# Performance work log

Hardware: AMD Instinct MI355X
Metric: run time of the kernel (lower is better)

The kernel has to match this reference:

```python
import jax, jax.numpy as jnp
import numpy as np

N = 100_000   # nodes
D = 64        # hidden = H * C
H, C = 8, 8   # heads, per-head channels
E = 500_000   # edges per edge set
EPS = 1e-3    # keras LayerNormalization default epsilon
RSQRT_C = np.float32(1.0 / np.sqrt(C))


def setup_inputs() -> dict:
    key = jax.random.key(0)
    ks = jax.random.split(key, 13)
    s = 0.05
    return dict(
        x=jax.random.normal(ks[0], (N, D), jnp.float32),
        src0=jax.random.randint(ks[1], (E,), 0, N, jnp.int32),
        dst0=jax.random.randint(ks[2], (E,), 0, N, jnp.int32),
        src1=jax.random.randint(ks[3], (E,), 0, N, jnp.int32),
        dst1=jax.random.randint(ks[4], (E,), 0, N, jnp.int32),
        Wk=jax.random.normal(ks[5], (D, D), jnp.float32) * s,
        bk=jnp.zeros((D,), jnp.float32),
        Wm=jax.random.normal(ks[6], (D, D), jnp.float32) * s,
        bm=jnp.zeros((D,), jnp.float32),
        Wq=jax.random.normal(ks[7], (D, D), jnp.float32) * s,
        bq=jnp.zeros((D,), jnp.float32),
        Wa=jax.random.normal(ks[8], (D, D), jnp.float32) * s,
        ba=jnp.zeros((D,), jnp.float32),
        Watt0=jax.random.normal(ks[9], (H, C, C), jnp.float32) * s,
        Wmsg0=jax.random.normal(ks[10], (H, C, C), jnp.float32) * s,
        prior0=jnp.ones((H,), jnp.float32),
        Watt1=jax.random.normal(ks[11], (H, C, C), jnp.float32) * s,
        Wmsg1=jax.random.normal(ks[12], (H, C, C), jnp.float32) * s,
        prior1=jnp.ones((H,), jnp.float32),
        skip_w=jnp.ones((1,), jnp.float32),
        ln_gamma=jnp.ones((D,), jnp.float32),
        ln_beta=jnp.zeros((D,), jnp.float32),
    )


def _edge_terms(k, m, q, src, dst, Watt, Wmsg, prior):
    # gather sender keys/messages, apply per-edge-set per-head projections
    ke = jnp.einsum('ehk,hkl->ehl', k[src], Watt)          # [E,H,C]
    score = jnp.einsum('ehc,ehc->eh', ke, q[dst]) * prior * RSQRT_C  # [E,H]
    me = jnp.einsum('ehk,hkl->ehl', m[src], Wmsg)          # [E,H,C]
    return score, me


def _forward(x, src0, dst0, src1, dst1, Wk, bk, Wm, bm, Wq, bq, Wa, ba,
             Watt0, Wmsg0, prior0, Watt1, Wmsg1, prior1,
             skip_w, ln_gamma, ln_beta):
    n = x.shape[0]
    split = lambda t: t.reshape(n, H, C)
    k = split(x @ Wk + bk)   # sender keys   [N,H,C]
    m = split(x @ Wm + bm)   # sender msgs   [N,H,C]
    q = split(x @ Wq + bq)   # receiver qrys [N,H,C]

    s0, m0 = _edge_terms(k, m, q, src0, dst0, Watt0, Wmsg0, prior0)
    s1, m1 = _edge_terms(k, m, q, src1, dst1, Watt1, Wmsg1, prior1)

    # joint segment softmax over ALL incoming edges per receiver (across edge sets)
    scores = jnp.concatenate([s0, s1], axis=0)  # [Et,H]
    msgs = jnp.concatenate([m0, m1], axis=0)    # [Et,H,C]
    recv = jnp.concatenate([dst0, dst1], axis=0)
    smax = jax.ops.segment_max(scores, recv, num_segments=n)
    ex = jnp.exp(scores - smax[recv])
    denom = jax.ops.segment_sum(ex, recv, num_segments=n)
    coef = ex / denom[recv]                      # [Et,H]

    pooled = jax.ops.segment_sum(coef[:, :, None] * msgs, recv, num_segments=n)  # [N,H,C]
    merged = pooled.reshape(n, D)
    agg = jax.nn.gelu(merged, approximate=False) @ Wa + ba
    # (dropout_rate=0.0 -> identity)
    sc = jax.nn.sigmoid(skip_w[0])               # learnable weighted skip
    out = sc * agg + (1.0 - sc) * x
    # layer norm (keras default eps=1e-3)
    mu = jnp.mean(out, axis=-1, keepdims=True)
    var = jnp.var(out, axis=-1, keepdims=True)
    return ln_gamma * (out - mu) * jax.lax.rsqrt(var + EPS) + ln_beta


def reference(x, src0, dst0, src1, dst1, Wk, bk, Wm, bm, Wq, bq, Wa, ba,
              Watt0, Wmsg0, prior0, Watt1, Wmsg1, prior1,
              skip_w, ln_gamma, ln_beta):
    return _forward(x, src0, dst0, src1, dst1, Wk, bk, Wm, bm, Wq, bq, Wa, ba,
                    Watt0, Wmsg0, prior0, Watt1, Wmsg1, prior1,
                    skip_w, ln_gamma, ln_beta)
```

## Files before the change

kernel.cpp:

```cpp
#include <hip/hip_runtime.h>
#include <hip/hip_fp16.h>
#include <cstdint>
#include <cstddef>

#define TPB 256
static constexpr float RSQRT_C_F = 0.35355339059327373f;

typedef __attribute__((ext_vector_type(8))) short bf16x8;
typedef __attribute__((ext_vector_type(4))) float f32x4;
typedef __attribute__((ext_vector_type(2))) float f32x2;

#if __has_builtin(__builtin_amdgcn_cvt_pk_f32_fp8) && __has_builtin(__builtin_amdgcn_cvt_pk_fp8_f32)
#define USE_HW_FP8 1
#endif

__device__ __forceinline__ unsigned short f2bf(float f) {
    unsigned u = __float_as_uint(f);
    u += 0x7FFFu + ((u >> 16) & 1u);
    return (unsigned short)(u >> 16);
}
__device__ __forceinline__ float bf2f(unsigned short h) {
    return __uint_as_float((unsigned)h << 16);
}
__device__ __forceinline__ float loF(unsigned u) { return __uint_as_float(u << 16); }
__device__ __forceinline__ float hiF(unsigned u) { return __uint_as_float(u); }

__device__ __forceinline__ unsigned char enc8(float v) {
#ifdef USE_HW_FP8
    return (unsigned char)(__builtin_amdgcn_cvt_pk_fp8_f32(v, v, 0, false) & 0xff);
#else
    unsigned s = (__float_as_uint(v) >> 24) & 0x80u;
    float a = fabsf(v);
    if (a < 0.015625f) {
        int m = __float2int_rn(a * 512.f);
        return (unsigned char)(s | (unsigned)m);
    }
    if (a > 448.f) return (unsigned char)(s | 0x7e);
    unsigned u = __float_as_uint(a);
    u += 0x7FFFFu + ((u >> 20) & 1u);
    unsigned e8 = ((u >> 23) & 0xffu) - 120u;
    unsigned m3 = (u >> 20) & 7u;
    if (e8 > 15u) return (unsigned char)(s | 0x7e);
    return (unsigned char)(s | (e8 << 3) | m3);
#endif
}

__device__ __forceinline__ void dec8x8(uint2 v, float* o) {
#ifdef USE_HW_FP8
    f32x2 a = __builtin_amdgcn_cvt_pk_f32_fp8((int)v.x, false);
    f32x2 b = __builtin_amdgcn_cvt_pk_f32_fp8((int)v.x, true);
    f32x2 c = __builtin_amdgcn_cvt_pk_f32_fp8((int)v.y, false);
    f32x2 d = __builtin_amdgcn_cvt_pk_f32_fp8((int)v.y, true);
    o[0] = a.x; o[1] = a.y; o[2] = b.x; o[3] = b.y;
    o[4] = c.x; o[5] = c.y; o[6] = d.x; o[7] = d.y;
#else
    unsigned w[2] = {v.x, v.y};
    #pragma unroll
    for (int i = 0; i < 8; i++) {
        unsigned bb = (w[i >> 2] >> ((i & 3) * 8)) & 0xffu;
        unsigned short hs = (unsigned short)(((bb & 0x80u) << 8) | ((bb & 0x7fu) << 7));
        __half h = *reinterpret_cast<__half*>(&hs);
        o[i] = 256.f * __half2float(h);
    }
#endif
}

__global__ void zero_sub(int4* __restrict__ p, int n4) {
    int i = blockIdx.x * TPB + threadIdx.x;
    int stride = gridDim.x * TPB;
    for (; i < n4; i += stride) p[i] = int4{0, 0, 0, 0};
}

__global__ void prep1_kernel(const float* __restrict__ Wq, const float* __restrict__ bq,
                             const float* __restrict__ Wk, const float* __restrict__ bk,
                             const float* __restrict__ Wm, const float* __restrict__ bm,
                             const float* __restrict__ Watt0, const float* __restrict__ prior0,
                             const float* __restrict__ Watt1, const float* __restrict__ prior1,
                             const float* __restrict__ Wmsg0, const float* __restrict__ Wmsg1,
                             float* __restrict__ Wbig, float* __restrict__ bbig) {
    int idx = blockIdx.x * TPB + threadIdx.x;
    if (idx < 64 * 320) {
        int i = idx / 320, col = idx % 320;
        float v;
        if (col < 64) {
            v = Wq[i * 64 + col];
        } else {
            int j = col - 64, set = j >> 6, l = j & 63, h = l >> 3, lc = l & 7;
            const float* Win = (set < 2) ? Wk : Wm;
            const float* T = (set == 0) ? Watt0 : (set == 1) ? Watt1 : (set == 2) ? Wmsg0 : Wmsg1;
            float scale = (set == 0) ? prior0[h] * RSQRT_C_F
                        : (set == 1) ? prior1[h] * RSQRT_C_F : 1.f;
            float acc = 0.f;
            #pragma unroll
            for (int c = 0; c < 8; c++) acc += Win[i * 64 + h * 8 + c] * T[h * 64 + c * 8 + lc];
            v = acc * scale;
        }
        Wbig[idx] = v;
    } else if (idx < 64 * 320 + 320) {
        int col = idx - 64 * 320;
        float v;
        if (col < 64) {
            v = bq[col];
        } else {
            int j = col - 64, set = j >> 6, l = j & 63, h = l >> 3, lc = l & 7;
            const float* bin = (set < 2) ? bk : bm;
            const float* T = (set == 0) ? Watt0 : (set == 1) ? Watt1 : (set == 2) ? Wmsg0 : Wmsg1;
            float scale = (set == 0) ? prior0[h] * RSQRT_C_F
                        : (set == 1) ? prior1[h] * RSQRT_C_F : 1.f;
            float acc = 0.f;
            #pragma unroll
            for (int c = 0; c < 8; c++) acc += bin[h * 8 + c] * T[h * 64 + c * 8 + lc];
            v = acc * scale;
        }
        bbig[col] = v;
    }
}

__global__ void prep2_kernel(const float* __restrict__ Wbig, const float* __restrict__ Wa,
                             unsigned short* __restrict__ Wpack,
                             unsigned short* __restrict__ Wapack) {
    int p = blockIdx.x * TPB + threadIdx.x;
    bool isWa = (p >= 40 * 64);
    if (p >= 48 * 64) return;
    int pl = isWa ? p - 40 * 64 : p;
    int lane = pl & 63, ctkt = pl >> 6;
    int ct = ctkt >> 1, kt = ctkt & 1;
    int kbase = kt * 32 + (lane >> 4) * 8;
    int col = ct * 16 + (lane & 15);
    const float* W = isWa ? Wa : Wbig;
    const int stride = isWa ? 64 : 320;
    unsigned short h[8];
    #pragma unroll
    for (int j = 0; j < 8; j++) h[j] = f2bf(W[(size_t)(kbase + j) * stride + col]);
    uint4 pk;
    pk.x = (unsigned)h[0] | ((unsigned)h[1] << 16);
    pk.y = (unsigned)h[2] | ((unsigned)h[3] << 16);
    pk.z = (unsigned)h[4] | ((unsigned)h[5] << 16);
    pk.w = (unsigned)h[6] | ((unsigned)h[7] << 16);
    unsigned short* dst = isWa ? Wapack : Wpack;
    *(uint4*)&dst[(size_t)pl * 8] = pk;
}

__global__ void hist_kernel(const int* __restrict__ dst0, const int* __restrict__ dst1,
                            int* __restrict__ sub, int* __restrict__ rank,
                            int E0, int Etot, int N) {
    const int gid = blockIdx.x * TPB + threadIdx.x;
    const int S = gridDim.x * TPB;
    #pragma unroll
    for (int k = 0; k < 4; k++) {
        int e = gid + k * S;
        if (e < Etot) {
            int d = (e < E0) ? dst0[e] : dst1[e - E0];
            d = min(max(d, 0), N - 1);
            rank[e] = atomicAdd(&sub[((e >> 8) & 7) * N + d], 1);
        }
    }
}

__global__ void scan1(int* __restrict__ sub, int* __restrict__ offsets,
                      int* __restrict__ blocksums, int n) {
    __shared__ int sums[TPB];
    int b = blockIdx.x, t = threadIdx.x;
    int base = b * 1024 + t * 4;
    int cnt[4];
    #pragma unroll
    for (int i = 0; i < 4; i++) {
        int d = base + i;
        int s = 0;
        if (d < n) {
            #pragma unroll
            for (int bb = 0; bb < 8; bb++) {
                int v = sub[bb * n + d];
                sub[bb * n + d] = s;
                s += v;
            }
        }
        cnt[i] = s;
    }
    int local = cnt[0] + cnt[1] + cnt[2] + cnt[3];
    sums[t] = local;
    __syncthreads();
    for (int off = 1; off < TPB; off <<= 1) {
        int add = (t >= off) ? sums[t - off] : 0;
        __syncthreads();
        sums[t] += add;
        __syncthreads();
    }
    int excl = sums[t] - local;
    if (base + 0 < n) offsets[base + 0] = excl;
    if (base + 1 < n) offsets[base + 1] = excl + cnt[0];
    if (base + 2 < n) offsets[base + 2] = excl + cnt[0] + cnt[1];
    if (base + 3 < n) offsets[base + 3] = excl + cnt[0] + cnt[1] + cnt[2];
    if (t == TPB - 1) blocksums[b] = sums[TPB - 1];
}

__global__ void scan2(int* __restrict__ blocksums, int nb) {
    __shared__ int s[TPB];
    int t = threadIdx.x;
    int v = (t < nb) ? blocksums[t] : 0;
    s[t] = v;
    __syncthreads();
    for (int off = 1; off < TPB; off <<= 1) {
        int add = (t >= off) ? s[t - off] : 0;
        __syncthreads();
        s[t] += add;
        __syncthreads();
    }
    if (t < nb) blocksums[t] = s[t] - v;
}

__global__ void scan3(int* __restrict__ offsets, const int* __restrict__ blocksums,
                      int* __restrict__ sub, int n, int Etot) {
    int i = blockIdx.x * TPB + threadIdx.x;
    if (i < n) {
        int v = offsets[i] + blocksums[i >> 10];
        offsets[i] = v;
        #pragma unroll
        for (int b = 0; b < 8; b++) sub[b * n + i] += v;
    }
    if (i == n) offsets[n] = Etot;
}

__global__ void scatter_kernel(const int* __restrict__ src0, const int* __restrict__ dst0,
                               const int* __restrict__ src1, const int* __restrict__ dst1,
                               const int* __restrict__ sub,
                               const int* __restrict__ rank, unsigned* __restrict__ records,
                               int E0, int Etot, int N) {
    const int gid = blockIdx.x * TPB + threadIdx.x;
    const int S = gridDim.x * TPB;
    #pragma unroll
    for (int k = 0; k < 4; k++) {
        int e = gid + k * S;
        if (e < Etot) {
            int s, d, setbit;
            if (e < E0) { s = src0[e]; d = dst0[e]; setbit = 0; }
            else        { s = src1[e - E0]; d = dst1[e - E0]; setbit = 1; }
            d = min(max(d, 0), N - 1);
            int pos = sub[((e >> 8) & 7) * N + d] + rank[e];
            pos = min(max(pos, 0), Etot - 1);
            records[pos] = (unsigned)s | ((unsigned)setbit << 24);
        }
    }
}

__global__ __launch_bounds__(TPB) void proj_mfma(const float* __restrict__ x,
                                                 const unsigned short* __restrict__ Wpack,
                                                 const float* __restrict__ bbig,
                                                 unsigned short* __restrict__ qbuf,
                                                 unsigned char* __restrict__ kmbuf8,
                                                 int N) {
    const int lane = threadIdx.x & 63;
    const int wv = threadIdx.x >> 6;
    const int rowbase = blockIdx.x * 64 + wv * 16;
    const int arow = min(rowbase + (lane & 15), N - 1);
    const int kbase = (lane >> 4) * 8;

    bf16x8 afrag[2];
    #pragma unroll
    for (int kt = 0; kt < 2; kt++) {
        const float* xp = x + (size_t)arow * 64 + kt * 32 + kbase;
        float4 v0 = *(const float4*)xp;
        float4 v1 = *(const float4*)(xp + 4);
        bf16x8 a;
        a[0] = (short)f2bf(v0.x); a[1] = (short)f2bf(v0.y);
        a[2] = (short)f2bf(v0.z); a[3] = (short)f2bf(v0.w);
        a[4] = (short)f2bf(v1.x); a[5] = (short)f2bf(v1.y);
        a[6] = (short)f2bf(v1.z); a[7] = (short)f2bf(v1.w);
        afrag[kt] = a;
    }

    const int colq = lane & 15;
    const int rgrp = (lane >> 4) * 4;

    for (int ct = 0; ct < 20; ct++) {
        bf16x8 b0 = *(const bf16x8*)(Wpack + ((size_t)(ct * 2 + 0) * 64 + lane) * 8);
        bf16x8 b1 = *(const bf16x8*)(Wpack + ((size_t)(ct * 2 + 1) * 64 + lane) * 8);
        f32x4 acc = {0.f, 0.f, 0.f, 0.f};
        acc = __builtin_amdgcn_mfma_f32_16x16x32_bf16(afrag[0], b0, acc, 0, 0, 0);
        acc = __builtin_amdgcn_mfma_f32_16x16x32_bf16(afrag[1], b1, acc, 0, 0, 0);
        const int col = ct * 16 + colq;
        const float bv = bbig[col];
        if (ct < 4) {
            #pragma unroll
            for (int r = 0; r < 4; r++) {
                int row = rowbase + rgrp + r;
                if (row < N) qbuf[(size_t)row * 64 + col] = f2bf(acc[r] + bv);
            }
        } else {
            const int cm = col - 64;
            #pragma unroll
            for (int r = 0; r < 4; r++) {
                int row = rowbase + rgrp + r;
                if (row < N) kmbuf8[(size_t)row * 256 + cm] = enc8(acc[r] + bv);
            }
        }
    }
}

__global__ __launch_bounds__(TPB) void pool_kernel(const unsigned short* __restrict__ qbuf,
                                                   const unsigned char* __restrict__ kmbuf8,
                                                   const unsigned* __restrict__ records,
                                                   const int* __restrict__ offsets,
                                                   unsigned short* __restrict__ pooledN,
                                                   int N) {
    const int lane = threadIdx.x & 63;
    const int j = lane & 7;
    const int r = ((blockIdx.x * TPB + threadIdx.x) >> 6) * 8 + (lane >> 3);
    if (r >= N) return;
    const int beg = offsets[r], end = offsets[r + 1];

    uint4 qv = *(const uint4*)(qbuf + (size_t)r * 64 + (j << 3));
    float qa0 = loF(qv.x), qa1 = hiF(qv.x), qa2 = loF(qv.y), qa3 = hiF(qv.y);
    float qa4 = loF(qv.z), qa5 = hiF(qv.z), qa6 = loF(qv.w), qa7 = hiF(qv.w);

    float d_run = 0.f;
    float p0 = 0.f, p1 = 0.f, p2 = 0.f, p3 = 0.f, p4 = 0.f, p5 = 0.f, p6 = 0.f, p7 = 0.f;

#define EDGE(T) {                                                              \
        unsigned rec = records[T];                                             \
        size_t base = ((size_t)(rec & 0xFFFFFFu) << 8) + (((rec >> 24) & 1u) << 6) + (j << 3); \
        uint2 kv = *(const uint2*)(kmbuf8 + base);                             \
        uint2 mv = *(const uint2*)(kmbuf8 + base + 128);                       \
        float kf[8], mf[8];                                                    \
        dec8x8(kv, kf); dec8x8(mv, mf);                                        \
        float s = kf[0] * qa0 + kf[1] * qa1 + kf[2] * qa2 + kf[3] * qa3        \
                + kf[4] * qa4 + kf[5] * qa5 + kf[6] * qa6 + kf[7] * qa7;       \
        float c = __expf(fminf(s, 60.f));                                      \
        d_run += c;                                                            \
        p0 += c * mf[0]; p1 += c * mf[1]; p2 += c * mf[2]; p3 += c * mf[3];    \
        p4 += c * mf[4]; p5 += c * mf[5]; p6 += c * mf[6]; p7 += c * mf[7];    \
    }

    int t = beg;
    for (; t + 1 < end; t += 2) { EDGE(t); EDGE(t + 1); }
    if (t < end) EDGE(t);
#undef EDGE

    const float inv = (end > beg) ? 1.f / d_run : 0.f;
    uint4 ov;
    ov.x = (unsigned)f2bf(p0 * inv) | ((unsigned)f2bf(p1 * inv) << 16);
    ov.y = (unsigned)f2bf(p2 * inv) | ((unsigned)f2bf(p3 * inv) << 16);
    ov.z = (unsigned)f2bf(p4 * inv) | ((unsigned)f2bf(p5 * inv) << 16);
    ov.w = (unsigned)f2bf(p6 * inv) | ((unsigned)f2bf(p7 * inv) << 16);
    *(uint4*)(pooledN + (size_t)r * 64 + (j << 3)) = ov;
}

__global__ __launch_bounds__(TPB) void final_mfma(const float* __restrict__ x,
                                                  const unsigned short* __restrict__ pooledN,
                                                  const unsigned short* __restrict__ Wapack,
                                                  const float* __restrict__ ba,
                                                  const float* __restrict__ skipw,
                                                  const float* __restrict__ gamma,
                                                  const float* __restrict__ beta,
                                                  float* __restrict__ out, int N) {
    const int lane = threadIdx.x & 63;
    const int wv = threadIdx.x >> 6;
    const int rowbase = blockIdx.x * 64 + wv * 16;
    const int arow = min(rowbase + (lane & 15), N - 1);
    const int kbase = (lane >> 4) * 8;
    const float sc = 1.f / (1.f + __expf(-skipw[0]));

    bf16x8 afrag[2];
    #pragma unroll
    for (int kt = 0; kt < 2; kt++) {
        uint4 pv = *(const uint4*)(pooledN + (size_t)arow * 64 + kt * 32 + kbase);
        float g[8];
        g[0] = loF(pv.x); g[1] = bf2f((unsigned short)(pv.x >> 16));
        g[2] = loF(pv.y); g[3] = bf2f((unsigned short)(pv.y >> 16));
        g[4] = loF(pv.z); g[5] = bf2f((unsigned short)(pv.z >> 16));
        g[6] = loF(pv.w); g[7] = bf2f((unsigned short)(pv.w >> 16));
        bf16x8 a;
        #pragma unroll
        for (int i = 0; i < 8; i++) {
            float gg = 0.5f * g[i] * (1.f + erff(g[i] * 0.70710678118654752f));
            a[i] = (short)f2bf(gg);
        }
        afrag[kt] = a;
    }

    const int colq = lane & 15;
    const int rgrp = (lane >> 4) * 4;

    float o[4][4];
    #pragma unroll
    for (int ct = 0; ct < 4; ct++) {
        bf16x8 b0 = *(const bf16x8*)(Wapack + ((size_t)(ct * 2 + 0) * 64 + lane) * 8);
        bf16x8 b1 = *(const bf16x8*)(Wapack + ((size_t)(ct * 2 + 1) * 64 + lane) * 8);
        f32x4 acc = {0.f, 0.f, 0.f, 0.f};
        acc = __builtin_amdgcn_mfma_f32_16x16x32_bf16(afrag[0], b0, acc, 0, 0, 0);
        acc = __builtin_amdgcn_mfma_f32_16x16x32_bf16(afrag[1], b1, acc, 0, 0, 0);
        const int col = ct * 16 + colq;
        const float bav = ba[col];
        #pragma unroll
        for (int r = 0; r < 4; r++) {
            int row = min(rowbase + rgrp + r, N - 1);
            float xv = x[(size_t)row * 64 + col];
            o[ct][r] = sc * (acc[r] + bav) + (1.f - sc) * xv;
        }
    }

    #pragma unroll
    for (int r = 0; r < 4; r++) {
        float s1 = o[0][r] + o[1][r] + o[2][r] + o[3][r];
        float s2 = o[0][r] * o[0][r] + o[1][r] * o[1][r]
                 + o[2][r] * o[2][r] + o[3][r] * o[3][r];
        #pragma unroll
        for (int off = 1; off <= 8; off <<= 1) {
            s1 += __shfl_xor(s1, off, 64);
            s2 += __shfl_xor(s2, off, 64);
        }
        float mu = s1 * (1.f / 64.f);
        float var = s2 * (1.f / 64.f) - mu * mu;
        float rs = rsqrtf(var + 1e-3f);
        const int row = rowbase + rgrp + r;
        if (row < N) {
            #pragma unroll
            for (int ct = 0; ct < 4; ct++) {
                const int col = ct * 16 + colq;
                out[(size_t)row * 64 + col] = gamma[col] * (o[ct][r] - mu) * rs + beta[col];
            }
        }
    }
}

extern "C" void kernel_launch(void* const* d_in, const int* in_sizes, int n_in,
                              void* d_out, int out_size, void* d_ws, size_t ws_size,
                              hipStream_t stream) {
    const float* x      = (const float*)d_in[0];
    const int*   src0   = (const int*)d_in[1];
    const int*   dst0   = (const int*)d_in[2];
    const int*   src1   = (const int*)d_in[3];
    const int*   dst1   = (const int*)d_in[4];
    const float* Wk     = (const float*)d_in[5];
    const float* bk     = (const float*)d_in[6];
    const float* Wm     = (const float*)d_in[7];
    const float* bm     = (const float*)d_in[8];
    const float* Wq     = (const float*)d_in[9];
    const float* bq     = (const float*)d_in[10];
    const float* Wa     = (const float*)d_in[11];
    const float* ba     = (const float*)d_in[12];
    const float* Watt0  = (const float*)d_in[13];
    const float* Wmsg0  = (const float*)d_in[14];
    const float* prior0 = (const float*)d_in[15];
    const float* Watt1  = (const float*)d_in[16];
    const float* Wmsg1  = (const float*)d_in[17];
    const float* prior1 = (const float*)d_in[18];
    const float* skipw  = (const float*)d_in[19];
    const float* gamma  = (const float*)d_in[20];
    const float* beta   = (const float*)d_in[21];

    const int N  = in_sizes[0] / 64;
    const int E0 = in_sizes[1];
    const int E1 = in_sizes[3];
    const int Etot = E0 + E1;

    float* ws       = (float*)d_ws;
    float* Wbig     = ws;
    float* bbig     = Wbig + 64 * 320;
    unsigned short* Wpack  = (unsigned short*)(bbig + 320);
    unsigned short* Wapack = Wpack + 40 * 64 * 8;
    unsigned short* qbuf   = Wapack + 8 * 64 * 8;
    unsigned short* pooledN = qbuf + (size_t)N * 64;
    unsigned char* kmbuf8  = (unsigned char*)(pooledN + (size_t)N * 64);
    int* sub        = (int*)(kmbuf8 + (size_t)N * 256);
    int* offsets    = sub + (size_t)8 * N;
    int* blocksums  = offsets + N + 1;
    int* rank       = blocksums + 512;
    unsigned* records = (unsigned*)(rank + Etot);

    const int nb1 = (N + 1023) / 1024;
    const int gE4 = (Etot + 4 * TPB - 1) / (4 * TPB);

    prep1_kernel<<<(64 * 320 + 320 + TPB - 1) / TPB, TPB, 0, stream>>>(
        Wq, bq, Wk, bk, Wm, bm, Watt0, prior0, Watt1, prior1, Wmsg0, Wmsg1, Wbig, bbig);
    zero_sub<<<1024, TPB, 0, stream>>>((int4*)sub, 2 * N);
    prep2_kernel<<<(48 * 64 + TPB - 1) / TPB, TPB, 0, stream>>>(Wbig, Wa, Wpack, Wapack);

    proj_mfma<<<(N + 63) / 64, TPB, 0, stream>>>(x, Wpack, bbig, qbuf, kmbuf8, N);

    hist_kernel<<<gE4, TPB, 0, stream>>>(dst0, dst1, sub, rank, E0, Etot, N);

    scan1<<<nb1, TPB, 0, stream>>>(sub, offsets, blocksums, N);
    scan2<<<1, TPB, 0, stream>>>(blocksums, nb1);
    scan3<<<(N + 1 + TPB - 1) / TPB, TPB, 0, stream>>>(offsets, blocksums, sub, N, Etot);

    scatter_kernel<<<gE4, TPB, 0, stream>>>(src0, dst0, src1, dst1, sub,
                                            rank, records, E0, Etot, N);

    pool_kernel<<<((size_t)N * 8 + TPB - 1) / TPB, TPB, 0, stream>>>(qbuf, kmbuf8, records,
                                                                     offsets, pooledN, N);

    final_mfma<<<(N + 63) / 64, TPB, 0, stream>>>(x, pooledN, Wapack, ba, skipw,
                                                  gamma, beta, (float*)d_out, N);
}
```

Baseline: 162.1 us.

## Fuse setup kernels, merge scan passes, and process two row tiles per projection block

```diff
diff --git a/kernel.cpp b/kernel.cpp
--- a/kernel.cpp
+++ b/kernel.cpp
@@ -65,39 +65,69 @@
 #endif
 }
 
-__global__ void zero_sub(int4* __restrict__ p, int n4) {
-    int i = blockIdx.x * TPB + threadIdx.x;
-    int stride = gridDim.x * TPB;
-    for (; i < n4; i += stride) p[i] = int4{0, 0, 0, 0};
-}
-
-__global__ void prep1_kernel(const float* __restrict__ Wq, const float* __restrict__ bq,
+__device__ __forceinline__ float wbig_elem(const float* __restrict__ Wq,
+                                           const float* __restrict__ Wk,
+                                           const float* __restrict__ Wm,
+                                           const float* __restrict__ Watt0,
+                                           const float* __restrict__ Watt1,
+                                           const float* __restrict__ Wmsg0,
+                                           const float* __restrict__ Wmsg1,
+                                           const float* __restrict__ prior0,
+                                           const float* __restrict__ prior1,
+                                           int i, int col) {
+    if (col < 64) return Wq[i * 64 + col];
+    int j = col - 64, set = j >> 6, l = j & 63, h = l >> 3, lc = l & 7;
+    const float* Win = (set < 2) ? Wk : Wm;
+    const float* T = (set == 0) ? Watt0 : (set == 1) ? Watt1 : (set == 2) ? Wmsg0 : Wmsg1;
+    float scale = (set == 0) ? prior0[h] * RSQRT_C_F
+                : (set == 1) ? prior1[h] * RSQRT_C_F : 1.f;
+    float acc = 0.f;
+    #pragma unroll
+    for (int c = 0; c < 8; c++) acc += Win[i * 64 + h * 8 + c] * T[h * 64 + c * 8 + lc];
+    return acc * scale;
+}
+
+__global__ void setup_kernel(const float* __restrict__ Wq, const float* __restrict__ bq,
                              const float* __restrict__ Wk, const float* __restrict__ bk,
                              const float* __restrict__ Wm, const float* __restrict__ bm,
                              const float* __restrict__ Watt0, const float* __restrict__ prior0,
                              const float* __restrict__ Watt1, const float* __restrict__ prior1,
                              const float* __restrict__ Wmsg0, const float* __restrict__ Wmsg1,
-                             float* __restrict__ Wbig, float* __restrict__ bbig) {
-    int idx = blockIdx.x * TPB + threadIdx.x;
-    if (idx < 64 * 320) {
-        int i = idx / 320, col = idx % 320;
-        float v;
-        if (col < 64) {
-            v = Wq[i * 64 + col];
+                             const float* __restrict__ Wa,
+                             float* __restrict__ bbig,
+                             unsigned short* __restrict__ Wpack,
+                             unsigned short* __restrict__ Wapack,
+                             int4* __restrict__ subzero, int n4) {
+    const int b = blockIdx.x, t = threadIdx.x;
+    if (b < 12) {
+        int p = b * TPB + t;
+        if (p >= 48 * 64) return;
+        bool isWa = (p >= 40 * 64);
+        int pl = isWa ? p - 40 * 64 : p;
+        int lane = pl & 63, ctkt = pl >> 6;
+        int ct = ctkt >> 1, kt = ctkt & 1;
+        int kbase = kt * 32 + (lane >> 4) * 8;
+        int col = ct * 16 + (lane & 15);
+        unsigned short h[8];
+        if (isWa) {
+            #pragma unroll
+            for (int j = 0; j < 8; j++) h[j] = f2bf(Wa[(size_t)(kbase + j) * 64 + col]);
         } else {
-            int j = col - 64, set = j >> 6, l = j & 63, h = l >> 3, lc = l & 7;
-            const float* Win = (set < 2) ? Wk : Wm;
-            const float* T = (set == 0) ? Watt0 : (set == 1) ? Watt1 : (set == 2) ? Wmsg0 : Wmsg1;
-            float scale = (set == 0) ? prior0[h] * RSQRT_C_F
-                        : (set == 1) ? prior1[h] * RSQRT_C_F : 1.f;
-            float acc = 0.f;
-            #pragma unroll
-            for (int c = 0; c < 8; c++) acc += Win[i * 64 + h * 8 + c] * T[h * 64 + c * 8 + lc];
-            v = acc * scale;
-        }
-        Wbig[idx] = v;
-    } else if (idx < 64 * 320 + 320) {
-        int col = idx - 64 * 320;
+            #pragma unroll
+            for (int j = 0; j < 8; j++)
+                h[j] = f2bf(wbig_elem(Wq, Wk, Wm, Watt0, Watt1, Wmsg0, Wmsg1,
+                                      prior0, prior1, kbase + j, col));
+        }
+        uint4 pk;
+        pk.x = (unsigned)h[0] | ((unsigned)h[1] << 16);
+        pk.y = (unsigned)h[2] | ((unsigned)h[3] << 16);
+        pk.z = (unsigned)h[4] | ((unsigned)h[5] << 16);
+        pk.w = (unsigned)h[6] | ((unsigned)h[7] << 16);
+        unsigned short* dst = isWa ? Wapack : Wpack;
+        *(uint4*)&dst[(size_t)pl * 8] = pk;
+    } else if (b < 14) {
+        int col = (b - 12) * TPB + t;
+        if (col >= 320) return;
         float v;
         if (col < 64) {
             v = bq[col];
@@ -113,32 +143,11 @@
             v = acc * scale;
         }
         bbig[col] = v;
-    }
-}
-
-__global__ void prep2_kernel(const float* __restrict__ Wbig, const float* __restrict__ Wa,
-                             unsigned short* __restrict__ Wpack,
-                             unsigned short* __restrict__ Wapack) {
-    int p = blockIdx.x * TPB + threadIdx.x;
-    bool isWa = (p >= 40 * 64);
-    if (p >= 48 * 64) return;
-    int pl = isWa ? p - 40 * 64 : p;
-    int lane = pl & 63, ctkt = pl >> 6;
-    int ct = ctkt >> 1, kt = ctkt & 1;
-    int kbase = kt * 32 + (lane >> 4) * 8;
-    int col = ct * 16 + (lane & 15);
-    const float* W = isWa ? Wa : Wbig;
-    const int stride = isWa ? 64 : 320;
-    unsigned short h[8];
-    #pragma unroll
-    for (int j = 0; j < 8; j++) h[j] = f2bf(W[(size_t)(kbase + j) * stride + col]);
-    uint4 pk;
-    pk.x = (unsigned)h[0] | ((unsigned)h[1] << 16);
-    pk.y = (unsigned)h[2] | ((unsigned)h[3] << 16);
-    pk.z = (unsigned)h[4] | ((unsigned)h[5] << 16);
-    pk.w = (unsigned)h[6] | ((unsigned)h[7] << 16);
-    unsigned short* dst = isWa ? Wapack : Wpack;
-    *(uint4*)&dst[(size_t)pl * 8] = pk;
+    } else {
+        int i = (b - 14) * TPB + t;
+        int stride = 18 * TPB;
+        for (; i < n4; i += stride) subzero[i] = int4{0, 0, 0, 0};
+    }
 }
 
 __global__ void hist_kernel(const int* __restrict__ dst0, const int* __restrict__ dst1,
@@ -194,8 +203,10 @@
     if (t == TPB - 1) blocksums[b] = sums[TPB - 1];
 }
 
-__global__ void scan2(int* __restrict__ blocksums, int nb) {
+__global__ void scan3(int* __restrict__ offsets, const int* __restrict__ blocksums,
+                      int* __restrict__ sub, int n, int Etot, int nb) {
     __shared__ int s[TPB];
+    __shared__ int excl[TPB];
     int t = threadIdx.x;
     int v = (t < nb) ? blocksums[t] : 0;
     s[t] = v;
@@ -206,17 +217,14 @@
         s[t] += add;
         __syncthreads();
     }
-    if (t < nb) blocksums[t] = s[t] - v;
-}
-
-__global__ void scan3(int* __restrict__ offsets, const int* __restrict__ blocksums,
-                      int* __restrict__ sub, int n, int Etot) {
-    int i = blockIdx.x * TPB + threadIdx.x;
+    excl[t] = s[t] - v;
+    __syncthreads();
+    int i = blockIdx.x * TPB + t;
     if (i < n) {
-        int v = offsets[i] + blocksums[i >> 10];
-        offsets[i] = v;
+        int vv = offsets[i] + excl[i >> 10];
+        offsets[i] = vv;
         #pragma unroll
-        for (int b = 0; b < 8; b++) sub[b * n + i] += v;
+        for (int b = 0; b < 8; b++) sub[b * n + i] += vv;
     }
     if (i == n) offsets[n] = Etot;
 }
@@ -251,14 +259,16 @@
                                                  int N) {
     const int lane = threadIdx.x & 63;
     const int wv = threadIdx.x >> 6;
-    const int rowbase = blockIdx.x * 64 + wv * 16;
-    const int arow = min(rowbase + (lane & 15), N - 1);
+    const int rb0 = blockIdx.x * 128 + wv * 16;
+    const int rb1 = rb0 + 64;
+    const int arow0 = min(rb0 + (lane & 15), N - 1);
+    const int arow1 = min(rb1 + (lane & 15), N - 1);
     const int kbase = (lane >> 4) * 8;
 
-    bf16x8 afrag[2];
+    bf16x8 afA[2], afB[2];
     #pragma unroll
     for (int kt = 0; kt < 2; kt++) {
-        const float* xp = x + (size_t)arow * 64 + kt * 32 + kbase;
+        const float* xp = x + (size_t)arow0 * 64 + kt * 32 + kbase;
         float4 v0 = *(const float4*)xp;
         float4 v1 = *(const float4*)(xp + 4);
         bf16x8 a;
@@ -266,7 +276,16 @@
         a[2] = (short)f2bf(v0.z); a[3] = (short)f2bf(v0.w);
         a[4] = (short)f2bf(v1.x); a[5] = (short)f2bf(v1.y);
         a[6] = (short)f2bf(v1.z); a[7] = (short)f2bf(v1.w);
-        afrag[kt] = a;
+        afA[kt] = a;
+        const float* xq = x + (size_t)arow1 * 64 + kt * 32 + kbase;
+        float4 w0 = *(const float4*)xq;
+        float4 w1 = *(const float4*)(xq + 4);
+        bf16x8 b;
+        b[0] = (short)f2bf(w0.x); b[1] = (short)f2bf(w0.y);
+        b[2] = (short)f2bf(w0.z); b[3] = (short)f2bf(w0.w);
+        b[4] = (short)f2bf(w1.x); b[5] = (short)f2bf(w1.y);
+        b[6] = (short)f2bf(w1.z); b[7] = (short)f2bf(w1.w);
+        afB[kt] = b;
     }
 
     const int colq = lane & 15;
@@ -275,23 +294,30 @@
     for (int ct = 0; ct < 20; ct++) {
         bf16x8 b0 = *(const bf16x8*)(Wpack + ((size_t)(ct * 2 + 0) * 64 + lane) * 8);
         bf16x8 b1 = *(const bf16x8*)(Wpack + ((size_t)(ct * 2 + 1) * 64 + lane) * 8);
-        f32x4 acc = {0.f, 0.f, 0.f, 0.f};
-        acc = __builtin_amdgcn_mfma_f32_16x16x32_bf16(afrag[0], b0, acc, 0, 0, 0);
-        acc = __builtin_amdgcn_mfma_f32_16x16x32_bf16(afrag[1], b1, acc, 0, 0, 0);
+        f32x4 accA = {0.f, 0.f, 0.f, 0.f};
+        accA = __builtin_amdgcn_mfma_f32_16x16x32_bf16(afA[0], b0, accA, 0, 0, 0);
+        accA = __builtin_amdgcn_mfma_f32_16x16x32_bf16(afA[1], b1, accA, 0, 0, 0);
+        f32x4 accB = {0.f, 0.f, 0.f, 0.f};
+        accB = __builtin_amdgcn_mfma_f32_16x16x32_bf16(afB[0], b0, accB, 0, 0, 0);
+        accB = __builtin_amdgcn_mfma_f32_16x16x32_bf16(afB[1], b1, accB, 0, 0, 0);
         const int col = ct * 16 + colq;
         const float bv = bbig[col];
         if (ct < 4) {
             #pragma unroll
             for (int r = 0; r < 4; r++) {
-                int row = rowbase + rgrp + r;
-                if (row < N) qbuf[(size_t)row * 64 + col] = f2bf(acc[r] + bv);
+                int row = rb0 + rgrp + r;
+                if (row < N) qbuf[(size_t)row * 64 + col] = f2bf(accA[r] + bv);
+                int row2 = rb1 + rgrp + r;
+                if (row2 < N) qbuf[(size_t)row2 * 64 + col] = f2bf(accB[r] + bv);
             }
         } else {
             const int cm = col - 64;
             #pragma unroll
             for (int r = 0; r < 4; r++) {
-                int row = rowbase + rgrp + r;
-                if (row < N) kmbuf8[(size_t)row * 256 + cm] = enc8(acc[r] + bv);
+                int row = rb0 + rgrp + r;
+                if (row < N) kmbuf8[(size_t)row * 256 + cm] = enc8(accA[r] + bv);
+                int row2 = rb1 + rgrp + r;
+                if (row2 < N) kmbuf8[(size_t)row2 * 256 + cm] = enc8(accB[r] + bv);
             }
         }
     }
@@ -455,8 +481,7 @@
     const int Etot = E0 + E1;
 
     float* ws       = (float*)d_ws;
-    float* Wbig     = ws;
-    float* bbig     = Wbig + 64 * 320;
+    float* bbig     = ws;
     unsigned short* Wpack  = (unsigned short*)(bbig + 320);
     unsigned short* Wapack = Wpack + 40 * 64 * 8;
     unsigned short* qbuf   = Wapack + 8 * 64 * 8;
@@ -471,18 +496,16 @@
     const int nb1 = (N + 1023) / 1024;
     const int gE4 = (Etot + 4 * TPB - 1) / (4 * TPB);
 
-    prep1_kernel<<<(64 * 320 + 320 + TPB - 1) / TPB, TPB, 0, stream>>>(
-        Wq, bq, Wk, bk, Wm, bm, Watt0, prior0, Watt1, prior1, Wmsg0, Wmsg1, Wbig, bbig);
-    zero_sub<<<1024, TPB, 0, stream>>>((int4*)sub, 2 * N);
-    prep2_kernel<<<(48 * 64 + TPB - 1) / TPB, TPB, 0, stream>>>(Wbig, Wa, Wpack, Wapack);
-
-    proj_mfma<<<(N + 63) / 64, TPB, 0, stream>>>(x, Wpack, bbig, qbuf, kmbuf8, N);
+    setup_kernel<<<32, TPB, 0, stream>>>(Wq, bq, Wk, bk, Wm, bm, Watt0, prior0,
+                                         Watt1, prior1, Wmsg0, Wmsg1, Wa,
+                                         bbig, Wpack, Wapack, (int4*)sub, 2 * N);
+
+    proj_mfma<<<(N + 127) / 128, TPB, 0, stream>>>(x, Wpack, bbig, qbuf, kmbuf8, N);
 
     hist_kernel<<<gE4, TPB, 0, stream>>>(dst0, dst1, sub, rank, E0, Etot, N);
 
     scan1<<<nb1, TPB, 0, stream>>>(sub, offsets, blocksums, N);
-    scan2<<<1, TPB, 0, stream>>>(blocksums, nb1);
-    scan3<<<(N + 1 + TPB - 1) / TPB, TPB, 0, stream>>>(offsets, blocksums, sub, N, Etot);
+    scan3<<<(N + 1 + TPB - 1) / TPB, TPB, 0, stream>>>(offsets, blocksums, sub, N, Etot, nb1);
 
     scatter_kernel<<<gE4, TPB, 0, stream>>>(src0, dst0, src1, dst1, sub,
                                             rank, records, E0, Etot, N);
```

Result: no change. 164.9 us (+1.8%).
